# Kernel optimization log

Hardware: AMD Instinct MI355X
Metric: run time of the kernel (lower is better)

Reference implementation:

```python
import jax, jax.numpy as jnp
import numpy as np

N, D, H, L = 16384, 512, 64, 7  # nodes, feature dim, hidden, num labels


def setup_inputs() -> dict:
    key = jax.random.key(0)
    ks = jax.random.split(key, 6)
    matrix = jax.random.randint(ks[0], (N, N), 0, 2).astype(jnp.float32)  # dense binary adjacency
    x_features = jax.random.normal(ks[1], (N, D), dtype=jnp.float32)
    x_labels = jax.random.randint(ks[2], (N, L), 0, 2).astype(jnp.int32)  # multi-hot labels
    W2 = jax.random.normal(ks[3], (D, H), dtype=jnp.float32) / np.float32(np.sqrt(D))
    b2 = jnp.zeros((H,), jnp.float32)
    Wp = jax.random.normal(ks[4], (D, L), dtype=jnp.float32) / np.float32(np.sqrt(D))
    bp = jnp.zeros((L,), jnp.float32)
    return {"matrix": matrix, "x_features": x_features, "W2": W2, "b2": b2,
            "Wp": Wp, "bp": bp, "x_labels": x_labels, "index": 123, "flag": 2}


def reference(matrix, x_features, W2, b2, Wp, bp, x_labels, index, flag):
    # Implements the flag != 1 path (trans2 -> labelwise aggregation -> maxpool -> predict).
    assert flag == 2
    z = x_features @ W2 + b2                      # [N, 64]  (trans2 over all nodes)
    row = matrix[index]                           # [N] binary neighbor mask of node `index`
    deg = matrix.sum(axis=1)                      # [N] degrees of all nodes
    # para_j = 1/sqrt(deg_j * deg_index) for neighbors, 0 otherwise (row is the mask)
    para = row / jnp.sqrt(deg * row.sum())        # [N]
    lab = x_labels.astype(z.dtype)                # [N, 7]
    # label-wise degree-normalized neighbor aggregation: tmp_a[i] = sum_j para_j * lab[j,i] * z[j]
    tmp_a = jnp.einsum('n,nl,nd->ld', para, lab, z)   # [7, 64]
    h = jax.nn.relu(jnp.concatenate([z[index], tmp_a.reshape(-1)])[None, :])  # [1, 512]
    # stack + MaxPool1d(2) over the pair == elementwise max
    h_combi = jnp.maximum(x_features[index][None, :], h)  # [1, 512]
    out = h_combi @ Wp + bp                        # [1, 7]
    return out
```

## Files before the change

### kernel.cpp

```cpp
#include <hip/hip_runtime.h>

#define NN 16384
#define DD 512
#define HH 64
#define LL 7
#define NAGG 256
#define JPB  (NN / NAGG)
#define DEGB 4096
#define RPB  (NN / DEGB)

typedef float f32x4 __attribute__((ext_vector_type(4)));

#define WS_QV 0
#define WS_S  16384
#define WS_CP 16400
#define WS_GP 20480

__global__ void k_deg(const float* __restrict__ matrix,
                      const int* __restrict__ pidx,
                      float* __restrict__ qv) {
    __shared__ float sdata[RPB][4];
    int t = threadIdx.x;
    int lane = t & 63;
    int wid = t >> 6;
    int idx = *pidx;
    int j0 = blockIdx.x;

    float gate[RPB];
    #pragma unroll
    for (int k = 0; k < RPB; ++k)
        gate[k] = matrix[(size_t)idx * NN + j0 + k * DEGB];

    float vsum[RPB];
    #pragma unroll
    for (int k = 0; k < RPB; ++k) vsum[k] = 0.f;

    #pragma unroll
    for (int k = 0; k < RPB; ++k) {
        if (gate[k] != 0.f) {
            const f32x4* r4 = (const f32x4*)(matrix + (size_t)(j0 + k * DEGB) * NN);
            float v0 = 0.f, v1 = 0.f, v2 = 0.f, v3 = 0.f;
            #pragma unroll
            for (int it = 0; it < 4; ++it) {
                f32x4 a  = __builtin_nontemporal_load(&r4[t + (it * 4 + 0) * 256]);
                f32x4 b  = __builtin_nontemporal_load(&r4[t + (it * 4 + 1) * 256]);
                f32x4 cc = __builtin_nontemporal_load(&r4[t + (it * 4 + 2) * 256]);
                f32x4 d  = __builtin_nontemporal_load(&r4[t + (it * 4 + 3) * 256]);
                v0 += a.x + a.y + a.z + a.w;
                v1 += b.x + b.y + b.z + b.w;
                v2 += cc.x + cc.y + cc.z + cc.w;
                v3 += d.x + d.y + d.z + d.w;
            }
            vsum[k] = (v0 + v1) + (v2 + v3);
        }
    }

    #pragma unroll
    for (int k = 0; k < RPB; ++k) {
        float v = vsum[k];
        #pragma unroll
        for (int off = 32; off > 0; off >>= 1)
            v += __shfl_down(v, off);
        if (lane == 0) sdata[k][wid] = v;
    }
    __syncthreads();
    if (t < RPB) {
        float deg = (sdata[t][0] + sdata[t][1]) + (sdata[t][2] + sdata[t][3]);
        qv[j0 + t * DEGB] = deg > 0.f ? rsqrtf(deg) : 0.f;
    }
}

__global__ void k_agg(const float* __restrict__ matrix,
                      const float* __restrict__ xf,
                      const int* __restrict__ lab,
                      const int* __restrict__ pidx,
                      const float* __restrict__ bp,
                      const float* __restrict__ qv,
                      float* __restrict__ gpart,
                      float* __restrict__ cpart,
                      float* __restrict__ Sout,
                      float* __restrict__ out) {
    __shared__ float sS[4];
    int t = threadIdx.x;
    int b = blockIdx.x;
    int d0 = t * 2;
    float2 acc[LL];
    #pragma unroll
    for (int l = 0; l < LL; ++l) acc[l] = make_float2(0.f, 0.f);
    float cacc[LL] = {0.f, 0.f, 0.f, 0.f, 0.f, 0.f, 0.f};

    #pragma unroll 1
    for (int trip = 0; trip < JPB / 8; ++trip) {
        int jj[8];
        float qq[8];
        #pragma unroll
        for (int k = 0; k < 8; ++k) {
            jj[k] = b + (trip * 8 + k) * NAGG;
            qq[k] = qv[jj[k]];
        }
        #pragma unroll
        for (int k = 0; k < 8; ++k) {
            if (qq[k] != 0.f) {
                float2 xv = *(const float2*)(xf + (size_t)jj[k] * DD + d0);
                float wl[LL];
                #pragma unroll
                for (int l = 0; l < LL; ++l)
                    wl[l] = qq[k] * (float)lab[jj[k] * LL + l];
                #pragma unroll
                for (int l = 0; l < LL; ++l) {
                    acc[l].x = fmaf(wl[l], xv.x, acc[l].x);
                    acc[l].y = fmaf(wl[l], xv.y, acc[l].y);
                }
                #pragma unroll
                for (int l = 0; l < LL; ++l) cacc[l] += wl[l];
            }
        }
    }
    #pragma unroll
    for (int l = 0; l < LL; ++l)
        *(float2*)(gpart + ((size_t)b * LL + l) * DD + d0) = acc[l];
    if (t == 0) {
        #pragma unroll
        for (int l = 0; l < LL; ++l) cpart[b * 8 + l] = cacc[l];
    }
    if (b == 0) {
        int idx = *pidx;
        const f32x4* r4 = (const f32x4*)(matrix + (size_t)idx * NN);
        float v = 0.f;
        #pragma unroll
        for (int it = 0; it < 16; ++it) {
            f32x4 a = r4[t + it * 256];
            v += a.x + a.y + a.z + a.w;
        }
        #pragma unroll
        for (int off = 32; off > 0; off >>= 1)
            v += __shfl_down(v, off);
        if ((t & 63) == 0) sS[t >> 6] = v;
        __syncthreads();
        if (t == 0) {
            Sout[0] = (sS[0] + sS[1]) + (sS[2] + sS[3]);
            #pragma unroll
            for (int l = 0; l < LL; ++l) out[l] = bp[l];
        }
    }
}

__global__ void k_final(const float* __restrict__ xf,
                        const float* __restrict__ W2,
                        const float* __restrict__ b2,
                        const float* __restrict__ Wp,
                        const int* __restrict__ pidx,
                        const float* __restrict__ gpart,
                        const float* __restrict__ cpart,
                        const float* __restrict__ Sf,
                        float* __restrict__ out) {
    __shared__ float glp[4][DD];
    __shared__ float gl[DD];
    __shared__ float csd[4];
    __shared__ float csum_s;
    __shared__ float out_acc[LL];
    int t = threadIdx.x;
    int b = blockIdx.x;
    int lane = t & 63;
    int wid = t >> 6;
    int idx = *pidx;

    if (b >= 1) {
        int l = b - 1;
        float2 s[4];
        #pragma unroll
        for (int q = 0; q < 4; ++q) s[q] = make_float2(0.f, 0.f);
        #pragma unroll 4
        for (int pbi = 0; pbi < NAGG / 4; ++pbi) {
            int pb = wid * (NAGG / 4) + pbi;
            const float* gb = gpart + ((size_t)pb * LL + l) * DD;
            #pragma unroll
            for (int q = 0; q < 4; ++q) {
                float2 v = *(const float2*)(gb + (lane + q * 64) * 2);
                s[q].x += v.x; s[q].y += v.y;
            }
        }
        #pragma unroll
        for (int q = 0; q < 4; ++q) {
            glp[wid][(lane + q * 64) * 2]     = s[q].x;
            glp[wid][(lane + q * 64) * 2 + 1] = s[q].y;
        }
        float cv = cpart[t * 8 + l];
        #pragma unroll
        for (int off = 32; off > 0; off >>= 1)
            cv += __shfl_down(cv, off);
        if (lane == 0) csd[wid] = cv;
    }
    if (t < LL) out_acc[t] = 0.f;
    __syncthreads();

    if (b >= 1) {
        gl[t * 2]     = ((glp[0][t * 2]     + glp[1][t * 2])
                       + (glp[2][t * 2]     + glp[3][t * 2]));
        gl[t * 2 + 1] = ((glp[0][t * 2 + 1] + glp[1][t * 2 + 1])
                       + (glp[2][t * 2 + 1] + glp[3][t * 2 + 1]));
        if (t == 0) csum_s = (csd[0] + csd[1]) + (csd[2] + csd[3]);
    }
    __syncthreads();

    int p = b * 64 + (t >> 2);
    int sub = t & 3;
    int h = (b == 0) ? p : (p - HH) & 63;
    int dbase = sub * 128;
    const float* src = (b == 0) ? (xf + (size_t)idx * DD) : gl;
    float s0 = 0.f, s1 = 0.f, s2 = 0.f, s3 = 0.f;
    #pragma unroll 8
    for (int d = 0; d < 128; d += 4) {
        s0 = fmaf(src[dbase + d],     W2[(dbase + d)     * HH + h], s0);
        s1 = fmaf(src[dbase + d + 1], W2[(dbase + d + 1) * HH + h], s1);
        s2 = fmaf(src[dbase + d + 2], W2[(dbase + d + 2) * HH + h], s2);
        s3 = fmaf(src[dbase + d + 3], W2[(dbase + d + 3) * HH + h], s3);
    }
    float v = (s0 + s1) + (s2 + s3);
    v += __shfl_down(v, 2);
    v += __shfl_down(v, 1);

    if (sub == 0) {
        float val;
        if (b == 0) {
            val = v + b2[p];
        } else {
            float sc = rsqrtf(Sf[0]);
            val = (v + csum_s * b2[h]) * sc;
        }
        float relu_v = val > 0.f ? val : 0.f;
        float hc = fmaxf(xf[(size_t)idx * DD + p], relu_v);
        #pragma unroll
        for (int o = 0; o < LL; ++o)
            atomicAdd(&out_acc[o], hc * Wp[p * LL + o]);
    }
    __syncthreads();
    if (t < LL) atomicAdd(&out[t], out_acc[t]);
}

extern "C" void kernel_launch(void* const* d_in, const int* in_sizes, int n_in,
                              void* d_out, int out_size, void* d_ws, size_t ws_size,
                              hipStream_t stream) {
    const float* matrix = (const float*)d_in[0];
    const float* xf     = (const float*)d_in[1];
    const float* W2     = (const float*)d_in[2];
    const float* b2     = (const float*)d_in[3];
    const float* Wp     = (const float*)d_in[4];
    const float* bp     = (const float*)d_in[5];
    const int*   lab    = (const int*)d_in[6];
    const int*   pidx   = (const int*)d_in[7];
    float* outp = (float*)d_out;
    float* wsf  = (float*)d_ws;

    k_deg<<<DEGB, 256, 0, stream>>>(matrix, pidx, wsf + WS_QV);
    k_agg<<<NAGG, 256, 0, stream>>>(matrix, xf, lab, pidx, bp, wsf + WS_QV,
                                    wsf + WS_GP, wsf + WS_CP, wsf + WS_S, outp);
    k_final<<<8, 256, 0, stream>>>(xf, W2, b2, Wp, pidx,
                                   wsf + WS_GP, wsf + WS_CP, wsf + WS_S, outp);
}
```

Measured before the change: 134.5 us.

## Use atomic work-stealing over 4-row chunks in degree kernel

The degree kernel now runs a persistent grid of 2048 blocks that repeatedly claim chunks of four consecutive rows through a global atomic counter, replacing the static mapping of four strided rows per block. Each block reads its four gate values as one vector load and sums only the rows that are neighbours of the indexed node. The aim is to balance the uneven, data-dependent row reads across compute units. It adds a memset launch, one atomic per chunk and extra block-wide barriers per chunk.

```diff
diff --git a/kernel.cpp b/kernel.cpp
--- a/kernel.cpp
+++ b/kernel.cpp
@@ -6,67 +6,76 @@
 #define LL 7
 #define NAGG 256
 #define JPB  (NN / NAGG)
-#define DEGB 4096
-#define RPB  (NN / DEGB)
+#define CHROWS 4
+#define NCHUNK (NN / CHROWS)
+#define DEGB 2048
 
 typedef float f32x4 __attribute__((ext_vector_type(4)));
 
-#define WS_QV 0
-#define WS_S  16384
-#define WS_CP 16400
-#define WS_GP 20480
+#define WS_QV  0
+#define WS_S   16384
+#define WS_CTR 16392
+#define WS_CP  16400
+#define WS_GP  20480
 
 __global__ void k_deg(const float* __restrict__ matrix,
                       const int* __restrict__ pidx,
-                      float* __restrict__ qv) {
-    __shared__ float sdata[RPB][4];
+                      float* __restrict__ qv,
+                      int* __restrict__ counter) {
+    __shared__ float sdata[CHROWS][4];
+    __shared__ int schunk;
     int t = threadIdx.x;
     int lane = t & 63;
     int wid = t >> 6;
     int idx = *pidx;
-    int j0 = blockIdx.x;
-
-    float gate[RPB];
-    #pragma unroll
-    for (int k = 0; k < RPB; ++k)
-        gate[k] = matrix[(size_t)idx * NN + j0 + k * DEGB];
-
-    float vsum[RPB];
-    #pragma unroll
-    for (int k = 0; k < RPB; ++k) vsum[k] = 0.f;
-
-    #pragma unroll
-    for (int k = 0; k < RPB; ++k) {
-        if (gate[k] != 0.f) {
-            const f32x4* r4 = (const f32x4*)(matrix + (size_t)(j0 + k * DEGB) * NN);
-            float v0 = 0.f, v1 = 0.f, v2 = 0.f, v3 = 0.f;
+    const f32x4* grow = (const f32x4*)(matrix + (size_t)idx * NN);
+
+    for (;;) {
+        if (t == 0) schunk = atomicAdd(counter, 1);
+        __syncthreads();
+        int c = schunk;
+        if (c >= NCHUNK) break;
+        int jbase = c * CHROWS;
+        f32x4 gate = grow[c];
+
+        float vsum[CHROWS];
+        #pragma unroll
+        for (int k = 0; k < CHROWS; ++k) vsum[k] = 0.f;
+
+        #pragma unroll
+        for (int k = 0; k < CHROWS; ++k) {
+            if (gate[k] != 0.f) {
+                const f32x4* r4 = (const f32x4*)(matrix + (size_t)(jbase + k) * NN);
+                float v0 = 0.f, v1 = 0.f, v2 = 0.f, v3 = 0.f;
+                #pragma unroll
+                for (int it = 0; it < 4; ++it) {
+                    f32x4 a  = __builtin_nontemporal_load(&r4[t + (it * 4 + 0) * 256]);
+                    f32x4 b  = __builtin_nontemporal_load(&r4[t + (it * 4 + 1) * 256]);
+                    f32x4 cc = __builtin_nontemporal_load(&r4[t + (it * 4 + 2) * 256]);
+                    f32x4 d  = __builtin_nontemporal_load(&r4[t + (it * 4 + 3) * 256]);
+                    v0 += a.x + a.y + a.z + a.w;
+                    v1 += b.x + b.y + b.z + b.w;
+                    v2 += cc.x + cc.y + cc.z + cc.w;
+                    v3 += d.x + d.y + d.z + d.w;
+                }
+                vsum[k] = (v0 + v1) + (v2 + v3);
+            }
+        }
+
+        #pragma unroll
+        for (int k = 0; k < CHROWS; ++k) {
+            float v = vsum[k];
             #pragma unroll
-            for (int it = 0; it < 4; ++it) {
-                f32x4 a  = __builtin_nontemporal_load(&r4[t + (it * 4 + 0) * 256]);
-                f32x4 b  = __builtin_nontemporal_load(&r4[t + (it * 4 + 1) * 256]);
-                f32x4 cc = __builtin_nontemporal_load(&r4[t + (it * 4 + 2) * 256]);
-                f32x4 d  = __builtin_nontemporal_load(&r4[t + (it * 4 + 3) * 256]);
-                v0 += a.x + a.y + a.z + a.w;
-                v1 += b.x + b.y + b.z + b.w;
-                v2 += cc.x + cc.y + cc.z + cc.w;
-                v3 += d.x + d.y + d.z + d.w;
-            }
-            vsum[k] = (v0 + v1) + (v2 + v3);
-        }
-    }
-
-    #pragma unroll
-    for (int k = 0; k < RPB; ++k) {
-        float v = vsum[k];
-        #pragma unroll
-        for (int off = 32; off > 0; off >>= 1)
-            v += __shfl_down(v, off);
-        if (lane == 0) sdata[k][wid] = v;
-    }
-    __syncthreads();
-    if (t < RPB) {
-        float deg = (sdata[t][0] + sdata[t][1]) + (sdata[t][2] + sdata[t][3]);
-        qv[j0 + t * DEGB] = deg > 0.f ? rsqrtf(deg) : 0.f;
+            for (int off = 32; off > 0; off >>= 1)
+                v += __shfl_down(v, off);
+            if (lane == 0) sdata[k][wid] = v;
+        }
+        __syncthreads();
+        if (t < CHROWS) {
+            float deg = (sdata[t][0] + sdata[t][1]) + (sdata[t][2] + sdata[t][3]);
+            qv[jbase + t] = deg > 0.f ? rsqrtf(deg) : 0.f;
+        }
+        __syncthreads();
     }
 }
 
@@ -252,7 +261,9 @@
     float* outp = (float*)d_out;
     float* wsf  = (float*)d_ws;
 
-    k_deg<<<DEGB, 256, 0, stream>>>(matrix, pidx, wsf + WS_QV);
+    hipMemsetAsync(wsf + WS_CTR, 0, sizeof(int), stream);
+    k_deg<<<DEGB, 256, 0, stream>>>(matrix, pidx, wsf + WS_QV,
+                                    (int*)(wsf + WS_CTR));
     k_agg<<<NAGG, 256, 0, stream>>>(matrix, xf, lab, pidx, bp, wsf + WS_QV,
                                     wsf + WS_GP, wsf + WS_CP, wsf + WS_S, outp);
     k_final<<<8, 256, 0, stream>>>(xf, W2, b2, Wp, pidx,
```

Result: slower. 165.0 us (+22.7%).
